# Kernel optimization log

Hardware: AMD Instinct MI355X
Metric: run time of the kernel (lower is better)

The kernel has to match this reference:

```python
import jax, jax.numpy as jnp
import numpy as np


def setup_inputs() -> dict:
    key = jax.random.key(0)
    k1, k2 = jax.random.split(key)
    mat_1 = jax.random.normal(k1, (8192, 128), dtype=jnp.float32)
    mat_2 = jax.random.normal(k2, (8192, 128), dtype=jnp.float32)
    return {"mat_1": mat_1, "mat_2": mat_2}


def reference(mat_1, mat_2):
    # Squared Euclidean distance between every row of mat_1 and every row of mat_2.
    # Same math as sum((mat_1[i] - mat_2[j])**2) but expressed via the
    # ||a||^2 + ||b||^2 - 2 a.b identity so the [n1, n2, d] intermediate is
    # never materialized (single GEMM + rank-1 broadcasts).
    sq1 = jnp.sum(mat_1 * mat_1, axis=1, keepdims=True)        # [n1, 1]
    sq2 = jnp.sum(mat_2 * mat_2, axis=1)                        # [n2]
    cross = jnp.einsum('id,jd->ij', mat_1, mat_2)               # [n1, n2]
    return sq1 + sq2[None, :] - 2.0 * cross
```

## Files before the change

kernel.cpp:

```cpp
#include <hip/hip_runtime.h>


typedef __attribute__((ext_vector_type(8))) short bf16x8;
typedef __attribute__((ext_vector_type(4))) float f32x4;

__device__ __forceinline__ short f2bf(float f) {
    union { float f; unsigned u; } x; x.f = f;
    unsigned r = x.u + 0x7FFFu + ((x.u >> 16) & 1u);
    return (short)(r >> 16);
}

__global__ void norms_kernel(const float* __restrict__ m1,
                             const float* __restrict__ m2,
                             float* __restrict__ n1,
                             float* __restrict__ n2,
                             int rows1, int rows2) {
    int gwave = (int)((blockIdx.x * blockDim.x + threadIdx.x) >> 6);
    int lane  = threadIdx.x & 63;
    const float* src;
    float* dst;
    int row;
    if (gwave < rows1) { src = m1; dst = n1; row = gwave; }
    else {
        row = gwave - rows1;
        if (row >= rows2) return;
        src = m2; dst = n2;
    }
    const float2* p = (const float2*)(src + (size_t)row * 128);
    float2 v = p[lane];
    float s = v.x * v.x + v.y * v.y;
#pragma unroll
    for (int off = 32; off; off >>= 1) s += __shfl_xor(s, off, 64);
    if (lane == 0) dst[row] = s;
}

#define BM 128
#define BN 128
#define BK 64

__global__ __launch_bounds__(256, 3)
void dist_kernel(const float* __restrict__ A, const float* __restrict__ B,
                 const float* __restrict__ n1, const float* __restrict__ n2,
                 float* __restrict__ out, int N2) {
    __shared__ short As[BM][BK];
    __shared__ short Bs[BN][BK];

    const int tid  = threadIdx.x;
    const int wave = tid >> 6;
    const int lane = tid & 63;
    const int q    = lane >> 4;
    const int l15  = lane & 15;

    const int ti = blockIdx.y * BM;
    const int tj = blockIdx.x * BN;

    const int wm = (wave >> 1) * 64;
    const int wn = (wave & 1) * 64;

    f32x4 acc[4][4] = {};

    for (int kc = 0; kc < 128; kc += BK) {
#pragma unroll
        for (int g = 0; g < 4; ++g) {
            int idx = tid + g * 256;
            int row = idx >> 3;
            int kg  = (idx & 7) * 8;
            const float4* pa = (const float4*)(A + (size_t)(ti + row) * 128 + kc + kg);
            float4 v0 = pa[0], v1 = pa[1];
            bf16x8 w;
            w[0] = f2bf(v0.x); w[1] = f2bf(v0.y); w[2] = f2bf(v0.z); w[3] = f2bf(v0.w);
            w[4] = f2bf(v1.x); w[5] = f2bf(v1.y); w[6] = f2bf(v1.z); w[7] = f2bf(v1.w);
            *(bf16x8*)&As[row][kg] = w;
        }
#pragma unroll
        for (int g = 0; g < 4; ++g) {
            int idx = tid + g * 256;
            int row = idx >> 3;
            int kg  = (idx & 7) * 8;
            const float4* pb = (const float4*)(B + (size_t)(tj + row) * 128 + kc + kg);
            float4 v0 = pb[0], v1 = pb[1];
            bf16x8 w;
            w[0] = f2bf(v0.x); w[1] = f2bf(v0.y); w[2] = f2bf(v0.z); w[3] = f2bf(v0.w);
            w[4] = f2bf(v1.x); w[5] = f2bf(v1.y); w[6] = f2bf(v1.z); w[7] = f2bf(v1.w);
            *(bf16x8*)&Bs[row][kg] = w;
        }
        __syncthreads();

#pragma unroll
        for (int kk = 0; kk < BK; kk += 32) {
            bf16x8 af[4], bfr[4];
#pragma unroll
            for (int mi = 0; mi < 4; ++mi)
                af[mi] = *(const bf16x8*)&As[wm + mi * 16 + l15][kk + q * 8];
#pragma unroll
            for (int ni = 0; ni < 4; ++ni)
                bfr[ni] = *(const bf16x8*)&Bs[wn + ni * 16 + l15][kk + q * 8];
#pragma unroll
            for (int mi = 0; mi < 4; ++mi)
#pragma unroll
                for (int ni = 0; ni < 4; ++ni)
                    acc[mi][ni] = __builtin_amdgcn_mfma_f32_16x16x32_bf16(
                        af[mi], bfr[ni], acc[mi][ni], 0, 0, 0);
        }
        __syncthreads();
    }

#pragma unroll
    for (int mi = 0; mi < 4; ++mi) {
        int r0 = ti + wm + mi * 16 + q * 4;
        float a0 = n1[r0 + 0], a1 = n1[r0 + 1], a2 = n1[r0 + 2], a3 = n1[r0 + 3];
#pragma unroll
        for (int ni = 0; ni < 4; ++ni) {
            int c = tj + wn + ni * 16 + l15;
            float nb = n2[c];
            f32x4 v = acc[mi][ni];
            out[(size_t)(r0 + 0) * N2 + c] = a0 + nb - 2.0f * v[0];
            out[(size_t)(r0 + 1) * N2 + c] = a1 + nb - 2.0f * v[1];
            out[(size_t)(r0 + 2) * N2 + c] = a2 + nb - 2.0f * v[2];
            out[(size_t)(r0 + 3) * N2 + c] = a3 + nb - 2.0f * v[3];
        }
    }
}

extern "C" void kernel_launch(void* const* d_in, const int* in_sizes, int n_in,
                              void* d_out, int out_size, void* d_ws, size_t ws_size,
                              hipStream_t stream) {
    const float* m1 = (const float*)d_in[0];
    const float* m2 = (const float*)d_in[1];
    float* out = (float*)d_out;
    const int rows1 = in_sizes[0] / 128;
    const int rows2 = in_sizes[1] / 128;

    float* n1 = (float*)d_ws;
    float* n2 = n1 + rows1;

    int total_waves = rows1 + rows2;
    int nb = (total_waves * 64 + 255) / 256;
    norms_kernel<<<nb, 256, 0, stream>>>(m1, m2, n1, n2, rows1, rows2);

    dim3 grid(rows2 / BN, rows1 / BM);
    dist_kernel<<<grid, 256, 0, stream>>>(m1, m2, n1, n2, out, rows2);
}
```

Before: 275.1 us.

## Precompute bf16 copies in prep kernel and load full-K tiles via global_load_lds

The norms kernel now also writes bf16 copies of both inputs to workspace. The distance kernel then loads the whole K=128 tile for A and B straight into LDS with direct global-to-LDS loads, using an XOR swizzle against bank conflicts. This removes the repeated fp32 loads and per-tile bf16 conversion across the 64x64 tile grid, and drops the inner K loop with its extra barriers. In exchange it adds a workspace write pass, uses 64 KB of LDS per block with lower occupancy, and falls back to the old kernel if the workspace is too small.

After: 276.3 us. About the same (+0.4%).

```diff
diff --git a/kernel.cpp b/kernel.cpp
--- a/kernel.cpp
+++ b/kernel.cpp
@@ -4,46 +4,54 @@
 typedef __attribute__((ext_vector_type(8))) short bf16x8;
 typedef __attribute__((ext_vector_type(4))) float f32x4;
 
-__device__ __forceinline__ short f2bf(float f) {
+__device__ __forceinline__ unsigned short f2bf(float f) {
     union { float f; unsigned u; } x; x.f = f;
     unsigned r = x.u + 0x7FFFu + ((x.u >> 16) & 1u);
-    return (short)(r >> 16);
-}
-
-__global__ void norms_kernel(const float* __restrict__ m1,
-                             const float* __restrict__ m2,
-                             float* __restrict__ n1,
-                             float* __restrict__ n2,
-                             int rows1, int rows2) {
+    return (unsigned short)(r >> 16);
+}
+
+__global__ void prep_kernel(const float* __restrict__ m1,
+                            const float* __restrict__ m2,
+                            float* __restrict__ n1,
+                            float* __restrict__ n2,
+                            unsigned short* __restrict__ abf,
+                            unsigned short* __restrict__ bbf,
+                            int rows1, int rows2) {
     int gwave = (int)((blockIdx.x * blockDim.x + threadIdx.x) >> 6);
     int lane  = threadIdx.x & 63;
     const float* src;
-    float* dst;
+    float* ndst;
+    unsigned short* bdst;
     int row;
-    if (gwave < rows1) { src = m1; dst = n1; row = gwave; }
+    if (gwave < rows1) { src = m1; ndst = n1; bdst = abf; row = gwave; }
     else {
         row = gwave - rows1;
         if (row >= rows2) return;
-        src = m2; dst = n2;
+        src = m2; ndst = n2; bdst = bbf;
     }
     const float2* p = (const float2*)(src + (size_t)row * 128);
     float2 v = p[lane];
     float s = v.x * v.x + v.y * v.y;
+    if (bdst) {
+        ushort2 w;
+        w.x = f2bf(v.x);
+        w.y = f2bf(v.y);
+        *(ushort2*)(bdst + (size_t)row * 128 + lane * 2) = w;
+    }
 #pragma unroll
     for (int off = 32; off; off >>= 1) s += __shfl_xor(s, off, 64);
-    if (lane == 0) dst[row] = s;
+    if (lane == 0) ndst[row] = s;
 }
 
 #define BM 128
 #define BN 128
-#define BK 64
-
-__global__ __launch_bounds__(256, 3)
-void dist_kernel(const float* __restrict__ A, const float* __restrict__ B,
+
+__global__ __launch_bounds__(256, 2)
+void dist_kernel(const unsigned short* __restrict__ Abf,
+                 const unsigned short* __restrict__ Bbf,
                  const float* __restrict__ n1, const float* __restrict__ n2,
                  float* __restrict__ out, int N2) {
-    __shared__ short As[BM][BK];
-    __shared__ short Bs[BN][BK];
+    __shared__ char lds[65536];
 
     const int tid  = threadIdx.x;
     const int wave = tid >> 6;
@@ -54,12 +62,100 @@
     const int ti = blockIdx.y * BM;
     const int tj = blockIdx.x * BN;
 
+    {
+        const char* Ab = (const char*)Abf + (size_t)ti * 256;
+        const char* Bb = (const char*)Bbf + (size_t)tj * 256;
+        const int rl = wave * 4 + (lane >> 4);
+        const int c  = (lane & 15) * 16;
+#pragma unroll
+        for (int it = 0; it < 8; ++it) {
+            int row = it * 16 + rl;
+            int sc  = c ^ ((row & 7) << 4);
+            __builtin_amdgcn_global_load_lds(
+                (const __attribute__((address_space(1))) void*)(Ab + (size_t)row * 256 + sc),
+                (__attribute__((address_space(3))) void*)(lds + it * 4096 + wave * 1024),
+                16, 0, 0);
+        }
+#pragma unroll
+        for (int it = 0; it < 8; ++it) {
+            int row = it * 16 + rl;
+            int sc  = c ^ ((row & 7) << 4);
+            __builtin_amdgcn_global_load_lds(
+                (const __attribute__((address_space(1))) void*)(Bb + (size_t)row * 256 + sc),
+                (__attribute__((address_space(3))) void*)(lds + 32768 + it * 4096 + wave * 1024),
+                16, 0, 0);
+        }
+    }
+    __syncthreads();
+
     const int wm = (wave >> 1) * 64;
     const int wn = (wave & 1) * 64;
 
     f32x4 acc[4][4] = {};
 
-    for (int kc = 0; kc < 128; kc += BK) {
+    const char* Abase = lds;
+    const char* Bbase = lds + 32768;
+#pragma unroll
+    for (int kk = 0; kk < 128; kk += 32) {
+        const int cb = kk * 2 + q * 16;
+        bf16x8 af[4], bfr[4];
+#pragma unroll
+        for (int mi = 0; mi < 4; ++mi) {
+            int row = wm + mi * 16 + l15;
+            af[mi] = *(const bf16x8*)(Abase + row * 256 + (cb ^ ((row & 7) << 4)));
+        }
+#pragma unroll
+        for (int ni = 0; ni < 4; ++ni) {
+            int row = wn + ni * 16 + l15;
+            bfr[ni] = *(const bf16x8*)(Bbase + row * 256 + (cb ^ ((row & 7) << 4)));
+        }
+#pragma unroll
+        for (int mi = 0; mi < 4; ++mi)
+#pragma unroll
+            for (int ni = 0; ni < 4; ++ni)
+                acc[mi][ni] = __builtin_amdgcn_mfma_f32_16x16x32_bf16(
+                    af[mi], bfr[ni], acc[mi][ni], 0, 0, 0);
+    }
+
+#pragma unroll
+    for (int mi = 0; mi < 4; ++mi) {
+        int r0 = ti + wm + mi * 16 + q * 4;
+        float a0 = n1[r0 + 0], a1 = n1[r0 + 1], a2 = n1[r0 + 2], a3 = n1[r0 + 3];
+#pragma unroll
+        for (int ni = 0; ni < 4; ++ni) {
+            int c = tj + wn + ni * 16 + l15;
+            float nb = n2[c];
+            f32x4 v = acc[mi][ni];
+            out[(size_t)(r0 + 0) * N2 + c] = a0 + nb - 2.0f * v[0];
+            out[(size_t)(r0 + 1) * N2 + c] = a1 + nb - 2.0f * v[1];
+            out[(size_t)(r0 + 2) * N2 + c] = a2 + nb - 2.0f * v[2];
+            out[(size_t)(r0 + 3) * N2 + c] = a3 + nb - 2.0f * v[3];
+        }
+    }
+}
+
+__global__ __launch_bounds__(256, 3)
+void dist_kernel_fb(const float* __restrict__ A, const float* __restrict__ B,
+                    const float* __restrict__ n1, const float* __restrict__ n2,
+                    float* __restrict__ out, int N2) {
+    __shared__ short As[128][64];
+    __shared__ short Bs[128][64];
+
+    const int tid  = threadIdx.x;
+    const int wave = tid >> 6;
+    const int lane = tid & 63;
+    const int q    = lane >> 4;
+    const int l15  = lane & 15;
+
+    const int ti = blockIdx.y * 128;
+    const int tj = blockIdx.x * 128;
+
+    const int wm = (wave >> 1) * 64;
+    const int wn = (wave & 1) * 64;
+
+    f32x4 acc[4][4] = {};
+
+    for (int kc = 0; kc < 128; kc += 64) {
 #pragma unroll
         for (int g = 0; g < 4; ++g) {
             int idx = tid + g * 256;
@@ -87,7 +183,7 @@
         __syncthreads();
 
 #pragma unroll
-        for (int kk = 0; kk < BK; kk += 32) {
+        for (int kk = 0; kk < 64; kk += 32) {
             bf16x8 af[4], bfr[4];
 #pragma unroll
             for (int mi = 0; mi < 4; ++mi)
@@ -131,13 +227,22 @@
     const int rows1 = in_sizes[0] / 128;
     const int rows2 = in_sizes[1] / 128;
 
+    const size_t need_norms = (size_t)(rows1 + rows2) * sizeof(float);
+    const size_t need_bf16  = (size_t)(rows1 + rows2) * 128 * sizeof(unsigned short);
+    const bool   fast       = ws_size >= need_norms + need_bf16;
+
     float* n1 = (float*)d_ws;
     float* n2 = n1 + rows1;
+    unsigned short* abf = fast ? (unsigned short*)(n2 + rows2) : nullptr;
+    unsigned short* bbf = fast ? abf + (size_t)rows1 * 128 : nullptr;
 
     int total_waves = rows1 + rows2;
     int nb = (total_waves * 64 + 255) / 256;
-    norms_kernel<<<nb, 256, 0, stream>>>(m1, m2, n1, n2, rows1, rows2);
+    prep_kernel<<<nb, 256, 0, stream>>>(m1, m2, n1, n2, abf, bbf, rows1, rows2);
 
     dim3 grid(rows2 / BN, rows1 / BM);
-    dist_kernel<<<grid, 256, 0, stream>>>(m1, m2, n1, n2, out, rows2);
-}
+    if (fast)
+        dist_kernel<<<grid, 256, 0, stream>>>(abf, bbf, n1, n2, out, rows2);
+    else
+        dist_kernel_fb<<<grid, 256, 0, stream>>>(m1, m2, n1, n2, out, rows2);
+}
```

## Load full K=128 tile once into swizzled LDS, drop inner K loop sync

Applied to the files above, without the earlier changes.

Stages the entire 128-wide K dimension of both A and B tiles into 64KB of LDS in a single pass, with an XOR swizzle on row index to avoid bank conflicts. This removes the two-iteration K loop and its barriers. It also swaps the manual bf16 rounding for the HIP intrinsic pair conversion. Occupancy drops from 3 to 2 blocks per CU because of the larger shared-memory footprint.

After: 276.7 us. No clear change (+0.6%).

```diff
diff --git a/kernel.cpp b/kernel.cpp
--- a/kernel.cpp
+++ b/kernel.cpp
@@ -1,14 +1,9 @@
 #include <hip/hip_runtime.h>
+#include <hip/hip_bf16.h>
 
 
 typedef __attribute__((ext_vector_type(8))) short bf16x8;
 typedef __attribute__((ext_vector_type(4))) float f32x4;
-
-__device__ __forceinline__ short f2bf(float f) {
-    union { float f; unsigned u; } x; x.f = f;
-    unsigned r = x.u + 0x7FFFu + ((x.u >> 16) & 1u);
-    return (short)(r >> 16);
-}
 
 __global__ void norms_kernel(const float* __restrict__ m1,
                              const float* __restrict__ m2,
@@ -36,14 +31,21 @@
 
 #define BM 128
 #define BN 128
-#define BK 64
 
-__global__ __launch_bounds__(256, 3)
+__device__ __forceinline__ bf16x8 cvt8(float4 v0, float4 v1) {
+    union { bf16x8 v; __hip_bfloat162 h[4]; } u;
+    u.h[0] = __float22bfloat162_rn(make_float2(v0.x, v0.y));
+    u.h[1] = __float22bfloat162_rn(make_float2(v0.z, v0.w));
+    u.h[2] = __float22bfloat162_rn(make_float2(v1.x, v1.y));
+    u.h[3] = __float22bfloat162_rn(make_float2(v1.z, v1.w));
+    return u.v;
+}
+
+__global__ __launch_bounds__(256, 2)
 void dist_kernel(const float* __restrict__ A, const float* __restrict__ B,
                  const float* __restrict__ n1, const float* __restrict__ n2,
                  float* __restrict__ out, int N2) {
-    __shared__ short As[BM][BK];
-    __shared__ short Bs[BN][BK];
+    __shared__ char lds[65536];
 
     const int tid  = threadIdx.x;
     const int wave = tid >> 6;
@@ -54,55 +56,53 @@
     const int ti = blockIdx.y * BM;
     const int tj = blockIdx.x * BN;
 
+#pragma unroll
+    for (int g = 0; g < 8; ++g) {
+        int idx = tid + g * 256;
+        int row = idx >> 4;
+        int ke  = (idx & 15) * 8;
+        int sw  = (ke * 2) ^ ((row & 7) << 4);
+        const float4* pa = (const float4*)(A + (size_t)(ti + row) * 128 + ke);
+        *(bf16x8*)(lds + row * 256 + sw) = cvt8(pa[0], pa[1]);
+    }
+#pragma unroll
+    for (int g = 0; g < 8; ++g) {
+        int idx = tid + g * 256;
+        int row = idx >> 4;
+        int ke  = (idx & 15) * 8;
+        int sw  = (ke * 2) ^ ((row & 7) << 4);
+        const float4* pb = (const float4*)(B + (size_t)(tj + row) * 128 + ke);
+        *(bf16x8*)(lds + 32768 + row * 256 + sw) = cvt8(pb[0], pb[1]);
+    }
+    __syncthreads();
+
     const int wm = (wave >> 1) * 64;
     const int wn = (wave & 1) * 64;
 
     f32x4 acc[4][4] = {};
 
-    for (int kc = 0; kc < 128; kc += BK) {
+    const char* Abase = lds;
+    const char* Bbase = lds + 32768;
 #pragma unroll
-        for (int g = 0; g < 4; ++g) {
-            int idx = tid + g * 256;
-            int row = idx >> 3;
-            int kg  = (idx & 7) * 8;
-            const float4* pa = (const float4*)(A + (size_t)(ti + row) * 128 + kc + kg);
-            float4 v0 = pa[0], v1 = pa[1];
-            bf16x8 w;
-            w[0] = f2bf(v0.x); w[1] = f2bf(v0.y); w[2] = f2bf(v0.z); w[3] = f2bf(v0.w);
-            w[4] = f2bf(v1.x); w[5] = f2bf(v1.y); w[6] = f2bf(v1.z); w[7] = f2bf(v1.w);
-            *(bf16x8*)&As[row][kg] = w;
+    for (int kk = 0; kk < 128; kk += 32) {
+        const int cb = kk * 2 + q * 16;
+        bf16x8 af[4], bfr[4];
+#pragma unroll
+        for (int mi = 0; mi < 4; ++mi) {
+            int row = wm + mi * 16 + l15;
+            af[mi] = *(const bf16x8*)(Abase + row * 256 + (cb ^ ((row & 7) << 4)));
         }
 #pragma unroll
-        for (int g = 0; g < 4; ++g) {
-            int idx = tid + g * 256;
-            int row = idx >> 3;
-            int kg  = (idx & 7) * 8;
-            const float4* pb = (const float4*)(B + (size_t)(tj + row) * 128 + kc + kg);
-            float4 v0 = pb[0], v1 = pb[1];
-            bf16x8 w;
-            w[0] = f2bf(v0.x); w[1] = f2bf(v0.y); w[2] = f2bf(v0.z); w[3] = f2bf(v0.w);
-            w[4] = f2bf(v1.x); w[5] = f2bf(v1.y); w[6] = f2bf(v1.z); w[7] = f2bf(v1.w);
-            *(bf16x8*)&Bs[row][kg] = w;
+        for (int ni = 0; ni < 4; ++ni) {
+            int row = wn + ni * 16 + l15;
+            bfr[ni] = *(const bf16x8*)(Bbase + row * 256 + (cb ^ ((row & 7) << 4)));
         }
-        __syncthreads();
-
 #pragma unroll
-        for (int kk = 0; kk < BK; kk += 32) {
-            bf16x8 af[4], bfr[4];
-#pragma unroll
-            for (int mi = 0; mi < 4; ++mi)
-                af[mi] = *(const bf16x8*)&As[wm + mi * 16 + l15][kk + q * 8];
+        for (int mi = 0; mi < 4; ++mi)
 #pragma unroll
             for (int ni = 0; ni < 4; ++ni)
-                bfr[ni] = *(const bf16x8*)&Bs[wn + ni * 16 + l15][kk + q * 8];
-#pragma unroll
-            for (int mi = 0; mi < 4; ++mi)
-#pragma unroll
-                for (int ni = 0; ni < 4; ++ni)
-                    acc[mi][ni] = __builtin_amdgcn_mfma_f32_16x16x32_bf16(
-                        af[mi], bfr[ni], acc[mi][ni], 0, 0, 0);
-        }
-        __syncthreads();
+                acc[mi][ni] = __builtin_amdgcn_mfma_f32_16x16x32_bf16(
+                    af[mi], bfr[ni], acc[mi][ni], 0, 0, 0);
     }
 
 #pragma unroll
```
